# Optimization experiments

Measured on AMD Instinct MI355X. Metric: run time of the kernel, lower is better.

The kernel has to match this reference:

```python
import jax, jax.numpy as jnp
import numpy as np

# ---- module hyperparameters (match BlurredNoise defaults) ----
CHANNELS = 1024
BLUR_WIDTHS = 128
NOISE_CHANNELS = CHANNELS // BLUR_WIDTHS  # 8
MIN_SR = 250.0
MAX_SR = 10000.0
CUTOFF = 2.0
WIDTH = 12.0
SR_BASE = 2.0
NORM_PER_FILTER = 1.0
KERNEL_SIZE = int(np.ceil(MAX_SR / 2))  # 5000

BATCH = 2
SEQ_LENGTH = 4096
IN_SEQ = SEQ_LENGTH + KERNEL_SIZE - 1  # 9095


def _kaiser_beta(a):
    # scipy.signal.kaiser_beta
    if a > 50:
        return 0.1102 * (a - 8.7)
    if a > 21:
        return 0.5842 * (a - 21) ** 0.4 + 0.07886 * (a - 21)
    return 0.0


def _firwin_lowpass(numtaps, cutoff, width, fs):
    # Re-implementation of scipy.signal.firwin(numtaps, cutoff, width=width, fs=fs)
    # (lowpass, pass_zero=True, Kaiser window chosen from transition width).
    nyq = 0.5 * fs
    atten = 2.285 * (numtaps - 1) * np.pi * (width / nyq) + 7.95  # kaiser_atten
    beta = _kaiser_beta(atten)
    win = np.kaiser(numtaps, beta)
    m = np.arange(numtaps) - (numtaps - 1) / 2.0
    right = cutoff / nyq
    h = right * np.sinc(right * m)  # ideal lowpass impulse response
    h = h * win
    h = h / h.sum()  # normalize DC gain to 1 (scale at f=0, pass_zero)
    return h.astype(np.float32)


def _build_filters():
    log_min = np.log(MIN_SR) / np.log(SR_BASE)
    log_max = np.log(MAX_SR) / np.log(SR_BASE)
    sampling_rates = SR_BASE ** np.linspace(log_min, log_max, BLUR_WIDTHS)
    sampling_rates = np.clip(sampling_rates, MIN_SR, MAX_SR)
    blur_filters = np.zeros((BLUR_WIDTHS, KERNEL_SIZE), dtype=np.float32)
    for i, sr in enumerate(sampling_rates):
        num_taps = int(np.ceil(sr / 2))
        blur_filters[i, -num_taps:] = _firwin_lowpass(num_taps, CUTOFF, WIDTH, sr)
    output_scale = 1.0 / np.sqrt((blur_filters ** 2).sum(axis=1))  # (128,)
    output_scale = output_scale.reshape(1, BLUR_WIDTHS, 1).astype(np.float32)
    return blur_filters, output_scale


def setup_inputs() -> dict:
    key = jax.random.key(0)
    noise = jax.random.normal(key, (BATCH, NOISE_CHANNELS, IN_SEQ), dtype=jnp.float32)
    bf, os_ = _build_filters()
    return {
        "noise": noise,
        "blur_filters": jnp.asarray(bf),
        "output_scale": jnp.asarray(os_),
    }


def reference(noise, blur_filters, output_scale):
    # noise: (n, c, t_in) with c = NOISE_CHANNELS
    n, c, t = noise.shape
    # einops.repeat 'n c t -> (n c) b t' followed by grouped conv (groups=b)
    # with per-group single input channel is exactly a standard conv with
    # 1 input channel and b output channels.
    x = noise.reshape(n * c, 1, t)                       # (n*c, 1, t_in)
    k = blur_filters[:, None, :]                         # (b, 1, K) OIW
    feats = jax.lax.conv_general_dilated(
        x, k, window_strides=(1,), padding="VALID",
        dimension_numbers=("NCH", "OIH", "NCH"))          # (n*c, b, T)
    feats = feats * (1.0 + NORM_PER_FILTER * (output_scale - 1.0))
    T = feats.shape[-1]
    # '(n c) b t -> n (c b) t'
    return feats.reshape(n, c * BLUR_WIDTHS, T)
```

## Files before the change

kernel.cpp:

```cpp
#include <hip/hip_runtime.h>
#include <hip/hip_bf16.h>


#define KS      5000
#define IN_SEQ  9095
#define T_OUT   4096
#define NBC     16
#define NF      128
#define SWZSTEP 352
#define CSTRIDE 1040
#define XBUF    (8*CSTRIDE)
#define FRONT   128
#define XPS     9312
#define SWZ_BYTES (4*SWZSTEP*1024)

typedef __attribute__((ext_vector_type(8)))  short v8s;
typedef __attribute__((ext_vector_type(4)))  float v4f;
typedef __attribute__((ext_vector_type(16))) float v16f;

__device__ __forceinline__ unsigned short f2b(float v) {
  union { __hip_bfloat16 h; unsigned short u; } cv;
  cv.h = __float2bfloat16(v);
  return cv.u;
}

__global__ void build_pre(const float* __restrict__ filt,
                          const float* __restrict__ noise,
                          unsigned short* __restrict__ swz,
                          float* __restrict__ xpad) {
  const int b = blockIdx.x;
  if (b < 352) {
    const int i = b * 256 + threadIdx.x;
    if (i >= 4 * SWZSTEP * 64) return;
    const int lane = i & 63;
    const int frag = i >> 6;
    const int ft = frag / SWZSTEP;
    const int s  = frag - ft * SWZSTEP;
    const int col = lane & 31;
    const int hi  = lane >> 5;
    const int jg0 = KS - 16 * (s + 1) + 8 * hi;
    const float* row = filt + (size_t)(ft * 32 + col) * KS;
    unsigned short o[8];
    #pragma unroll
    for (int j = 0; j < 8; ++j) {
      int jg = jg0 + j;
      int jc = jg < 0 ? 0 : jg;
      float v = (jg >= 0 && jg < KS) ? row[jc] : 0.0f;
      o[j] = f2b(v);
    }
    *(uint4*)(swz + (((size_t)(ft * SWZSTEP + s)) << 9) + (lane << 3)) = *(uint4*)o;
  } else {
    const int i = (b - 352) * 256 + threadIdx.x;
    if (i >= NBC * XPS) return;
    const int r = i / XPS;
    const int pcol = i - r * XPS;
    const int lg = pcol - FRONT;
    xpad[i] = (lg >= 0 && lg < IN_SEQ) ? noise[r * IN_SEQ + lg] : 0.0f;
  }
}

template<int W, int UB, int D>
__device__ __forceinline__ void run_roll(
    const char* __restrict__ swzg, const float* __restrict__ xn,
    char* xw, int xrd_off, int t0, int lane, int sb0, int iters,
    v16f (&acc)[2][4])
{
  v8s breg[D][W];
  v8s areg[4][2];

  const char* sp[W];
  #pragma unroll
  for (int w = 0; w < W; ++w)
    sp[w] = swzg + (((size_t)((4 - W + w) * SWZSTEP + sb0)) << 10) + 16 * lane;

  auto stage = [&](char* buf, int sb) {
    const int wb = t0 + KS - 16 * (sb + UB);
    float4 xr[4];
    #pragma unroll
    for (int ii = 0; ii < 4; ++ii)
      xr[ii] = *(const float4*)(xn + (wb + 8 * lane + 4 * ii));
    const float* f = (const float*)xr;
    unsigned u8v[8];
    #pragma unroll
    for (int j = 0; j < 8; ++j)
      u8v[j] = (unsigned)f2b(f[2 * j]) | ((unsigned)f2b(f[2 * j + 1]) << 16);
    auto AL = [](unsigned hi, unsigned lo) { return (lo >> 16) | (hi << 16); };
    char* bufl = buf + 16 * lane;
    #pragma unroll
    for (int c = 0; c < 8; ++c) {
      const int h = c >> 1;
      uint4 wv;
      if ((c & 1) == 0)
        wv = (uint4){u8v[h], u8v[h + 1], u8v[h + 2], u8v[h + 3]};
      else
        wv = (uint4){AL(u8v[h + 1], u8v[h]),     AL(u8v[h + 2], u8v[h + 1]),
                     AL(u8v[h + 3], u8v[h + 2]), AL(u8v[h + 4], u8v[h + 3])};
      *(uint4*)(bufl + c * CSTRIDE) = wv;
    }
  };

  stage(xw, sb0);
  #pragma unroll
  for (int d = 0; d < D; ++d)
    #pragma unroll
    for (int w = 0; w < W; ++w)
      breg[d][w] = *(const v8s*)(sp[w] + (d << 10));
  {
    const char* xrd0 = xw + xrd_off;
    #pragma unroll
    for (int j = 0; j < 2; ++j)
      #pragma unroll
      for (int m = 0; m < 2; ++m)
        areg[j][m] = *(const v8s*)(xrd0 + 64 * m + 32 * (UB - 1 - j));
  }

  #pragma unroll 1
  for (int g = 0; g < iters; ++g) {
    char* bufn = xw + (((g + 1) & 1) ? XBUF : 0);
    const char* xrd  = xw + ((g & 1) ? XBUF : 0) + xrd_off;
    const char* xrdn = bufn + xrd_off;
    const int sbn = sb0 + UB * ((g + 1 < iters) ? g + 1 : g);
    stage(bufn, sbn);
    #pragma unroll
    for (int ii = 0; ii < UB; ++ii) {
      {
        const char* pn = (ii + 2 < UB) ? xrd : xrdn;
        const int off = (ii + 2 < UB) ? 32 * (UB - 3 - ii) : 32 * (2 * UB - 3 - ii);
        #pragma unroll
        for (int m = 0; m < 2; ++m)
          areg[(ii + 2) & 3][m] = *(const v8s*)(pn + 64 * m + off);
      }
      #pragma unroll
      for (int w = 0; w < W; ++w)
        #pragma unroll
        for (int m = 0; m < 2; ++m)
          acc[m][4 - W + w] = __builtin_amdgcn_mfma_f32_32x32x16_bf16(
              areg[ii & 3][m], breg[ii % D][w], acc[m][4 - W + w], 0, 0, 0);
      #pragma unroll
      for (int w = 0; w < W; ++w)
        breg[ii % D][w] = *(const v8s*)(sp[w] + ((ii + D) << 10));
    }
    #pragma unroll
    for (int w = 0; w < W; ++w) sp[w] += (UB << 10);
  }
}

__global__ __launch_bounds__(128, 2) void blur_mfma(
    const float* __restrict__ xpad,
    const unsigned short* __restrict__ swz,
    const float* __restrict__ scale,
    float* __restrict__ out)
{
  __shared__ __align__(16) char xb[2 * 2 * XBUF];
  const int tid  = threadIdx.x;
  const int lane = tid & 63;
  const int wid  = tid >> 6;
  const int b  = blockIdx.x;
  const int bc = b >> 6;
  const int t0 = (b & 63) << 6;
  const int row = lane & 31, hi = lane >> 5;
  const float* __restrict__ xn = xpad + (size_t)bc * XPS + FRONT;
  const char* swzg = (const char*)swz;
  char* xw = xb + wid * (2 * XBUF);
  const int xrd_off = (row & 7) * CSTRIDE + 16 * (row >> 3) + 16 * hi;

  v16f acc[2][4];
  #pragma unroll
  for (int m = 0; m < 2; ++m)
    #pragma unroll
    for (int n = 0; n < 4; ++n)
      #pragma unroll
      for (int j = 0; j < 16; ++j) acc[m][n][j] = 0.0f;

  if (wid == 0) {
    run_roll<4, 24,  3>(swzg, xn, xw, xrd_off, t0, lane,   0, 1, acc);
    run_roll<3, 16,  4>(swzg, xn, xw, xrd_off, t0, lane,  24, 2, acc);
  }
  run_roll<2, 24,  6>(swzg, xn, xw, xrd_off, t0, lane,
                      wid ? 104 : 56, wid ? 1 : 2, acc);
  if (wid == 1)
    run_roll<1, 24, 12>(swzg, xn, xw, xrd_off, t0, lane, 128, 8, acc);

  __syncthreads();
  #pragma unroll
  for (int mm = 0; mm < 2; ++mm) {
    if (wid == 1) {
      #pragma unroll
      for (int n = 0; n < 4; ++n)
        #pragma unroll
        for (int r2 = 0; r2 < 4; ++r2) {
          v4f v = {acc[mm][n][4 * r2],     acc[mm][n][4 * r2 + 1],
                   acc[mm][n][4 * r2 + 2], acc[mm][n][4 * r2 + 3]};
          *(v4f*)(xb + ((n * 4 + r2) << 10) + 16 * lane) = v;
        }
    }
    __syncthreads();
    if (wid == 0) {
      #pragma unroll
      for (int n = 0; n < 4; ++n)
        #pragma unroll
        for (int r2 = 0; r2 < 4; ++r2) {
          v4f v = *(const v4f*)(xb + ((n * 4 + r2) << 10) + 16 * lane);
          acc[mm][n][4 * r2]     += v[0];
          acc[mm][n][4 * r2 + 1] += v[1];
          acc[mm][n][4 * r2 + 2] += v[2];
          acc[mm][n][4 * r2 + 3] += v[3];
        }
    }
    __syncthreads();
  }

  if (wid == 0) {
    #pragma unroll
    for (int m = 0; m < 2; ++m)
      #pragma unroll
      for (int n = 0; n < 4; ++n) {
        const int F = 32 * n + row;
        const float sc = scale[F];
        float* op = out + (size_t)(bc * NF + F) * T_OUT + t0 + 32 * m + 4 * hi;
        #pragma unroll
        for (int r2 = 0; r2 < 4; ++r2) {
          v4f o = {acc[m][n][4 * r2] * sc, acc[m][n][4 * r2 + 1] * sc,
                   acc[m][n][4 * r2 + 2] * sc, acc[m][n][4 * r2 + 3] * sc};
          *(v4f*)(op + 8 * r2) = o;
        }
      }
  }
}

extern "C" void kernel_launch(void* const* d_in, const int* in_sizes, int n_in,
                              void* d_out, int out_size, void* d_ws, size_t ws_size,
                              hipStream_t stream) {
  const float* noise = (const float*)d_in[0];
  const float* filt  = (const float*)d_in[1];
  const float* scale = (const float*)d_in[2];
  float* out = (float*)d_out;

  unsigned short* swz = (unsigned short*)d_ws;
  float* xpad = (float*)((char*)d_ws + SWZ_BYTES);

  const int pad_blocks = (NBC * XPS + 255) / 256;
  build_pre<<<352 + pad_blocks, 256, 0, stream>>>(filt, noise, swz, xpad);
  blur_mfma<<<1024, 128, 0, stream>>>(xpad, swz, scale, out);
}
```

Baseline: 113.2 us.

## Read A fragments from pre-shifted bf16 global copies instead of LDS staging

The preprocessing kernel now writes four bf16 copies of the padded noise, each shifted by one sample, so that every MFMA A-fragment can be loaded straight from global memory with 8-byte loads. This removes the per-iteration LDS staging (fp32 load, bf16 convert, shifted shared-memory writes) and the double buffering in the main loop. The work split between the two waves is also rebalanced with a different unroll for the W=2 segment. In exchange the kernel issues more global/L2 loads per MFMA and writes a larger preprocessed buffer.

```diff
diff --git a/kernel.cpp b/kernel.cpp
--- a/kernel.cpp
+++ b/kernel.cpp
@@ -8,10 +8,9 @@
 #define NBC     16
 #define NF      128
 #define SWZSTEP 352
-#define CSTRIDE 1040
-#define XBUF    (8*CSTRIDE)
-#define FRONT   128
-#define XPS     9312
+#define FRONT   192
+#define XPS2    9344
+#define CS      (NBC*XPS2)
 #define SWZ_BYTES (4*SWZSTEP*1024)
 
 typedef __attribute__((ext_vector_type(8)))  short v8s;
@@ -27,7 +26,7 @@
 __global__ void build_pre(const float* __restrict__ filt,
                           const float* __restrict__ noise,
                           unsigned short* __restrict__ swz,
-                          float* __restrict__ xpad) {
+                          unsigned short* __restrict__ xb16) {
   const int b = blockIdx.x;
   if (b < 352) {
     const int i = b * 256 + threadIdx.x;
@@ -51,19 +50,21 @@
     *(uint4*)(swz + (((size_t)(ft * SWZSTEP + s)) << 9) + (lane << 3)) = *(uint4*)o;
   } else {
     const int i = (b - 352) * 256 + threadIdx.x;
-    if (i >= NBC * XPS) return;
-    const int r = i / XPS;
-    const int pcol = i - r * XPS;
-    const int lg = pcol - FRONT;
-    xpad[i] = (lg >= 0 && lg < IN_SEQ) ? noise[r * IN_SEQ + lg] : 0.0f;
+    if (i >= 4 * CS) return;
+    const int p   = i / CS;
+    const int rem = i - p * CS;
+    const int r   = rem / XPS2;
+    const int col = rem - r * XPS2;
+    const int lg  = col - FRONT + p;
+    const float v = (lg >= 0 && lg < IN_SEQ) ? noise[r * IN_SEQ + lg] : 0.0f;
+    xb16[i] = f2b(v);
   }
 }
 
 template<int W, int UB, int D>
 __device__ __forceinline__ void run_roll(
-    const char* __restrict__ swzg, const float* __restrict__ xn,
-    char* xw, int xrd_off, int t0, int lane, int sb0, int iters,
-    v16f (&acc)[2][4])
+    const char* __restrict__ swzg, const char* __restrict__ abase,
+    int lane, int sb0, int iters, v16f (&acc)[2][4])
 {
   v8s breg[D][W];
   v8s areg[4][2];
@@ -73,62 +74,31 @@
   for (int w = 0; w < W; ++w)
     sp[w] = swzg + (((size_t)((4 - W + w) * SWZSTEP + sb0)) << 10) + 16 * lane;
 
-  auto stage = [&](char* buf, int sb) {
-    const int wb = t0 + KS - 16 * (sb + UB);
-    float4 xr[4];
-    #pragma unroll
-    for (int ii = 0; ii < 4; ++ii)
-      xr[ii] = *(const float4*)(xn + (wb + 8 * lane + 4 * ii));
-    const float* f = (const float*)xr;
-    unsigned u8v[8];
-    #pragma unroll
-    for (int j = 0; j < 8; ++j)
-      u8v[j] = (unsigned)f2b(f[2 * j]) | ((unsigned)f2b(f[2 * j + 1]) << 16);
-    auto AL = [](unsigned hi, unsigned lo) { return (lo >> 16) | (hi << 16); };
-    char* bufl = buf + 16 * lane;
-    #pragma unroll
-    for (int c = 0; c < 8; ++c) {
-      const int h = c >> 1;
-      uint4 wv;
-      if ((c & 1) == 0)
-        wv = (uint4){u8v[h], u8v[h + 1], u8v[h + 2], u8v[h + 3]};
-      else
-        wv = (uint4){AL(u8v[h + 1], u8v[h]),     AL(u8v[h + 2], u8v[h + 1]),
-                     AL(u8v[h + 3], u8v[h + 2]), AL(u8v[h + 4], u8v[h + 3])};
-      *(uint4*)(bufl + c * CSTRIDE) = wv;
-    }
-  };
-
-  stage(xw, sb0);
+  const char* ap = abase - 32 * sb0;
+
   #pragma unroll
   for (int d = 0; d < D; ++d)
     #pragma unroll
     for (int w = 0; w < W; ++w)
       breg[d][w] = *(const v8s*)(sp[w] + (d << 10));
-  {
-    const char* xrd0 = xw + xrd_off;
-    #pragma unroll
-    for (int j = 0; j < 2; ++j)
-      #pragma unroll
-      for (int m = 0; m < 2; ++m)
-        areg[j][m] = *(const v8s*)(xrd0 + 64 * m + 32 * (UB - 1 - j));
-  }
+  #pragma unroll
+  for (int j = 0; j < 3; ++j)
+    #pragma unroll
+    for (int m = 0; m < 2; ++m) {
+      *(uint2*)&areg[j][m]       = *(const uint2*)(ap - 32 * j + 64 * m);
+      *((uint2*)&areg[j][m] + 1) = *(const uint2*)(ap - 32 * j + 64 * m + 8);
+    }
 
   #pragma unroll 1
   for (int g = 0; g < iters; ++g) {
-    char* bufn = xw + (((g + 1) & 1) ? XBUF : 0);
-    const char* xrd  = xw + ((g & 1) ? XBUF : 0) + xrd_off;
-    const char* xrdn = bufn + xrd_off;
-    const int sbn = sb0 + UB * ((g + 1 < iters) ? g + 1 : g);
-    stage(bufn, sbn);
     #pragma unroll
     for (int ii = 0; ii < UB; ++ii) {
-      {
-        const char* pn = (ii + 2 < UB) ? xrd : xrdn;
-        const int off = (ii + 2 < UB) ? 32 * (UB - 3 - ii) : 32 * (2 * UB - 3 - ii);
-        #pragma unroll
-        for (int m = 0; m < 2; ++m)
-          areg[(ii + 2) & 3][m] = *(const v8s*)(pn + 64 * m + off);
+      #pragma unroll
+      for (int m = 0; m < 2; ++m) {
+        *(uint2*)&areg[(ii + 3) & 3][m] =
+            *(const uint2*)(ap - 32 * (ii + 3) + 64 * m);
+        *((uint2*)&areg[(ii + 3) & 3][m] + 1) =
+            *(const uint2*)(ap - 32 * (ii + 3) + 64 * m + 8);
       }
       #pragma unroll
       for (int w = 0; w < W; ++w)
@@ -142,16 +112,17 @@
     }
     #pragma unroll
     for (int w = 0; w < W; ++w) sp[w] += (UB << 10);
+    ap -= 32 * UB;
   }
 }
 
 __global__ __launch_bounds__(128, 2) void blur_mfma(
-    const float* __restrict__ xpad,
+    const unsigned short* __restrict__ xb16,
     const unsigned short* __restrict__ swz,
     const float* __restrict__ scale,
     float* __restrict__ out)
 {
-  __shared__ __align__(16) char xb[2 * 2 * XBUF];
+  __shared__ __align__(16) char xb[16384];
   const int tid  = threadIdx.x;
   const int lane = tid & 63;
   const int wid  = tid >> 6;
@@ -159,10 +130,11 @@
   const int bc = b >> 6;
   const int t0 = (b & 63) << 6;
   const int row = lane & 31, hi = lane >> 5;
-  const float* __restrict__ xn = xpad + (size_t)bc * XPS + FRONT;
   const char* swzg = (const char*)swz;
-  char* xw = xb + wid * (2 * XBUF);
-  const int xrd_off = (row & 7) * CSTRIDE + 16 * (row >> 3) + 16 * hi;
+  const int p = row & 3;
+  const char* abase = (const char*)xb16 +
+      2 * ((size_t)p * CS + (size_t)bc * XPS2 +
+           (FRONT + (row - p) + 8 * hi + t0 + KS - 16));
 
   v16f acc[2][4];
   #pragma unroll
@@ -173,13 +145,13 @@
       for (int j = 0; j < 16; ++j) acc[m][n][j] = 0.0f;
 
   if (wid == 0) {
-    run_roll<4, 24,  3>(swzg, xn, xw, xrd_off, t0, lane,   0, 1, acc);
-    run_roll<3, 16,  4>(swzg, xn, xw, xrd_off, t0, lane,  24, 2, acc);
-  }
-  run_roll<2, 24,  6>(swzg, xn, xw, xrd_off, t0, lane,
-                      wid ? 104 : 56, wid ? 1 : 2, acc);
-  if (wid == 1)
-    run_roll<1, 24, 12>(swzg, xn, xw, xrd_off, t0, lane, 128, 8, acc);
+    run_roll<4, 24,  3>(swzg, abase, lane,   0, 1, acc);
+    run_roll<3, 16,  4>(swzg, abase, lane,  24, 2, acc);
+    run_roll<2, 12,  6>(swzg, abase, lane,  56, 5, acc);
+  } else {
+    run_roll<2, 12,  6>(swzg, abase, lane, 116, 1, acc);
+    run_roll<1, 24, 12>(swzg, abase, lane, 128, 8, acc);
+  }
 
   __syncthreads();
   #pragma unroll
@@ -236,10 +208,10 @@
   const float* scale = (const float*)d_in[2];
   float* out = (float*)d_out;
 
-  unsigned short* swz = (unsigned short*)d_ws;
-  float* xpad = (float*)((char*)d_ws + SWZ_BYTES);
-
-  const int pad_blocks = (NBC * XPS + 255) / 256;
-  build_pre<<<352 + pad_blocks, 256, 0, stream>>>(filt, noise, swz, xpad);
-  blur_mfma<<<1024, 128, 0, stream>>>(xpad, swz, scale, out);
-}
+  unsigned short* swz  = (unsigned short*)d_ws;
+  unsigned short* xb16 = (unsigned short*)((char*)d_ws + SWZ_BYTES);
+
+  const int x_blocks = (4 * CS + 255) / 256;
+  build_pre<<<352 + x_blocks, 256, 0, stream>>>(filt, noise, swz, xb16);
+  blur_mfma<<<1024, 128, 0, stream>>>(xb16, swz, scale, out);
+}
```

After: 137.4 us. +21.4%, slower.
